# Performance work log

Measured on AMD Instinct MI355X. Metric: run time of the kernel, lower is better.

## Reference

```python
import jax, jax.numpy as jnp
import numpy as np

HEADS = 8
DIM_HEAD = 64
SCALE = DIM_HEAD ** -0.5


def setup_inputs() -> dict:
    key = jax.random.key(0)
    k1, k2, k3, k4 = jax.random.split(key, 4)
    b, dim, l = 4, 256, 2048
    hidden = HEADS * DIM_HEAD  # 512
    x = jax.random.normal(k1, (b, dim, l), dtype=jnp.float32)
    w_qkv = jax.random.normal(k2, (3 * hidden, dim), dtype=jnp.float32) * (dim ** -0.5)
    w_out = jax.random.normal(k3, (dim, hidden), dtype=jnp.float32) * (hidden ** -0.5)
    b_out = jax.random.normal(k4, (dim,), dtype=jnp.float32) * 0.01
    return {"x": x, "w_qkv": w_qkv, "w_out": w_out, "b_out": b_out}


def reference(x, w_qkv, w_out, b_out):
    b, c, l = x.shape
    hidden = HEADS * DIM_HEAD
    # 1x1 conv == pointwise linear over channels
    qkv = jnp.einsum('oc,bcl->bol', w_qkv, x)  # [b, 3*hidden, l]
    q, k, v = jnp.split(qkv, 3, axis=1)
    def to_heads(t):
        return t.reshape(b, HEADS, DIM_HEAD, l)  # b h d l
    q, k, v = to_heads(q), to_heads(k), to_heads(v)
    q = q * SCALE
    sim = jnp.einsum('bhdi,bhdj->bhij', q, k)      # [b, h, l, l]
    attn = jax.nn.softmax(sim, axis=-1)
    out = jnp.einsum('bhij,bhdj->bhid', attn, v)   # [b, h, l, d]
    out = out.transpose(0, 1, 3, 2).reshape(b, hidden, l)  # b (h d) l
    return jnp.einsum('oc,bcl->bol', w_out, out) + b_out[None, :, None]
```

## Files before the change

kernel.cpp:

```cpp
#include <hip/hip_runtime.h>
#include <math.h>

#define Bn   4
#define Cc   256
#define Ll   2048
#define Hh   8
#define Dd   64
#define HID  512
#define OQKV 1536

#define QSCALE 0.18033688011112042f
#define ESHIFT 4.328085122666891f

typedef _Float16 half4v __attribute__((ext_vector_type(4)));
typedef _Float16 half8v __attribute__((ext_vector_type(8)));
typedef __fp16   fp16x2 __attribute__((ext_vector_type(2)));
typedef float    f32x16 __attribute__((ext_vector_type(16)));
typedef unsigned uint2v __attribute__((ext_vector_type(2)));

__device__ __forceinline__ void gload_lds16(const _Float16* g, _Float16* l) {
  __builtin_amdgcn_global_load_lds(
      (const __attribute__((address_space(1))) void*)g,
      (__attribute__((address_space(3))) void*)l, 16, 0, 0);
}

__device__ inline unsigned pkrtz(float a, float b) {
  union { fp16x2 h; unsigned u; } v;
  v.h = __builtin_amdgcn_cvt_pkrtz(a, b);
  return v.u;
}

__global__ __launch_bounds__(256) void conv_xTw(const float* __restrict__ x,
                                                const float* __restrict__ wqkv,
                                                const float* __restrict__ wout,
                                                _Float16* __restrict__ xT,
                                                _Float16* __restrict__ wqkvh,
                                                _Float16* __restrict__ wouth) {
  __shared__ _Float16 T[64][72];
  const int l0 = blockIdx.x * 64, c0 = blockIdx.y * 64, bz = blockIdx.z;
  const int t = threadIdx.x;
  {
    int gid = (((blockIdx.z * gridDim.y + blockIdx.y) * gridDim.x + blockIdx.x) << 8) + t;
    int nthr = (gridDim.x * gridDim.y * gridDim.z) << 8;
    for (int i = gid; i < OQKV * Cc; i += nthr) {
      float v = wqkv[i];
      if (i < HID * Cc) v *= QSCALE;
      wqkvh[i] = (_Float16)v;
    }
    for (int i = gid; i < Cc * HID; i += nthr) wouth[i] = (_Float16)wout[i];
  }
  const float* xb = x + ((size_t)bz * Cc + c0) * Ll + l0;
  {
    int cl = t >> 2, lq = (t & 3) * 16;
#pragma unroll
    for (int i = 0; i < 16; i += 4) {
      float4 v = *(const float4*)&xb[(size_t)cl * Ll + lq + i];
      T[lq + i + 0][cl] = (_Float16)v.x;
      T[lq + i + 1][cl] = (_Float16)v.y;
      T[lq + i + 2][cl] = (_Float16)v.z;
      T[lq + i + 3][cl] = (_Float16)v.w;
    }
  }
  __syncthreads();
  {
    int ll = t >> 2, cq = (t & 3) * 16;
    _Float16* dst = xT + ((size_t)bz * Ll + l0 + ll) * Cc + c0 + cq;
    *(half8v*)&dst[0] = *(const half8v*)&T[ll][cq];
    *(half8v*)&dst[8] = *(const half8v*)&T[ll][cq + 8];
  }
}

template <int MODE>
__global__ __launch_bounds__(256) void gemm64(
    const _Float16* __restrict__ A, const _Float16* __restrict__ B,
    const float* __restrict__ bias, void* __restrict__ C, int M, int K) {
  __shared__ _Float16 As[64][64];
  __shared__ _Float16 Bs[64][64];
  const int bz = blockIdx.z;
  const int m0 = blockIdx.y * 64, n0 = blockIdx.x * 64;
  const int t = threadIdx.x;
  const int w = t >> 6, lane = t & 63, lid = lane & 31, lh = lane >> 5;
  const int mw = (w >> 1) * 32, nw = (w & 1) * 32;
  const _Float16* Bb = B + (size_t)bz * (size_t)Ll * K;
  const int srow = lane >> 3;
  const int sgr  = ((lane & 7) ^ srow) << 3;

  f32x16 acc;
#pragma unroll
  for (int r = 0; r < 16; ++r) acc[r] = 0.0f;

  for (int k0 = 0; k0 < K; k0 += 64) {
#pragma unroll
    for (int q = 0; q < 2; ++q) {
      const int r0 = (q * 4 + w) * 8;
      gload_lds16(&A[(size_t)(m0 + r0 + srow) * K + k0 + sgr], &As[r0][0]);
      gload_lds16(&Bb[(size_t)(n0 + r0 + srow) * K + k0 + sgr], &Bs[r0][0]);
    }
    __syncthreads();
    const int rk = lid & 7;
#pragma unroll
    for (int kq = 0; kq < 4; ++kq) {
      const int co = ((2 * kq + lh) ^ rk) << 3;
      half8v af = *(const half8v*)&As[mw + lid][co];
      half8v bf = *(const half8v*)&Bs[nw + lid][co];
      acc = __builtin_amdgcn_mfma_f32_32x32x16_f16(af, bf, acc, 0, 0, 0);
    }
    __syncthreads();
  }
#pragma unroll
  for (int r = 0; r < 16; ++r) {
    const int row = m0 + mw + (r & 3) + 8 * (r >> 2) + 4 * lh;
    const int col = n0 + nw + lid;
    if (MODE == 1) {
      ((float*)C)[((size_t)bz * M + row) * Ll + col] = acc[r] + bias[row];
    } else {
      ((_Float16*)C)[((size_t)bz * M + row) * Ll + col] = (_Float16)acc[r];
    }
  }
}

__global__ __launch_bounds__(512, 4) void attn_f16(const _Float16* __restrict__ qkv,
                                                   _Float16* __restrict__ aoutT) {
  const int n = blockIdx.x;
  const int xcd = n & 7;
  const int x = (n >> 3) & 15;
  const int gs = n >> 7;
  const int g = gs * 8 + xcd;
  const int h = g & 7, b = g >> 3;
  const int i0 = x * 128;

  const int t = threadIdx.x;
  const int w = t >> 6, lane = t & 63, lid = lane & 31, lh = lane >> 5;
  const int wg = w & 3;
  const int wj = w >> 2;
  const _Float16* qb = qkv + ((size_t)b * OQKV + h * Dd) * Ll;
  const _Float16* kb = qb + (size_t)HID * Ll;
  const _Float16* vb = qb + (size_t)(2 * HID) * Ll;

  __shared__ __align__(16) char lds_raw[55296];
  _Float16 (*Qs)[72]     = (_Float16 (*)[72])(lds_raw);
  _Float16 (*Ks)[64][72] = (_Float16 (*)[64][72])(lds_raw + 18432);
  _Float16 (*Vs)[64][72] = (_Float16 (*)[64][72])(lds_raw + 36864);

  {
    int il = ((t >> 8) << 6) + (t & 15) * 4;
    int dl = ((t >> 4) & 15) * 4;
    int cc = dl >> 3, cs = dl & 7;
    half4v rows[4];
#pragma unroll
    for (int r = 0; r < 4; ++r)
      rows[r] = *(const half4v*)&qb[(size_t)(dl + r) * Ll + i0 + il];
#pragma unroll
    for (int c = 0; c < 4; ++c) {
      half4v o;
      o[0] = rows[0][c]; o[1] = rows[1][c]; o[2] = rows[2][c]; o[3] = rows[3][c];
      int row = il + c;
      *(half4v*)&Qs[row][((cc ^ ((row >> 2) & 7)) << 3) | cs] = o;
    }
  }

  const bool isK = t < 256;
  const int ts = isK ? t : t - 256;
  const int kjl = (ts & 15) * 4, kdl = (ts >> 4) * 4;
  const int kcc = kdl >> 3, kcs = kdl & 7;
  const int vdl = ts >> 2, vjl = (ts & 3) * 16;

  if (isK) {
    half4v rows[4];
#pragma unroll
    for (int r = 0; r < 4; ++r)
      rows[r] = *(const half4v*)&kb[(size_t)(kdl + r) * Ll + kjl];
#pragma unroll
    for (int c = 0; c < 4; ++c) {
      half4v o;
      o[0] = rows[0][c]; o[1] = rows[1][c]; o[2] = rows[2][c]; o[3] = rows[3][c];
      int row = kjl + c;
      *(half4v*)&Ks[0][row][((kcc ^ ((row >> 2) & 7)) << 3) | kcs] = o;
    }
  } else {
    *(half8v*)&Vs[0][vdl][vjl]     = *(const half8v*)&vb[(size_t)vdl * Ll + vjl];
    *(half8v*)&Vs[0][vdl][vjl + 8] = *(const half8v*)&vb[(size_t)vdl * Ll + vjl + 8];
  }
  __syncthreads();

  const int key = (lid >> 2) & 7;
  half8v qf[4];
#pragma unroll
  for (int kq = 0; kq < 4; ++kq)
    qf[kq] = *(const half8v*)&Qs[32 * wg + lid][((2 * kq + lh) ^ key) << 3];

  float lsum = 0.0f;
  f32x16 oacc[2];
#pragma unroll
  for (int ds = 0; ds < 2; ++ds)
#pragma unroll
    for (int r = 0; r < 16; ++r) oacc[ds][r] = 0.0f;

  const int krow = wj * 32 + lid;

  for (int j0 = 0; j0 < Ll; j0 += 64) {
    const int cur = (j0 >> 6) & 1;
    const int nj = j0 + 64;
    const bool more = nj < Ll;

    half4v krows[4];
    half8v vr0, vr1;
    if (more) {
      if (isK) {
#pragma unroll
        for (int r = 0; r < 4; ++r)
          krows[r] = *(const half4v*)&kb[(size_t)(kdl + r) * Ll + nj + kjl];
      } else {
        vr0 = *(const half8v*)&vb[(size_t)vdl * Ll + nj + vjl];
        vr1 = *(const half8v*)&vb[(size_t)vdl * Ll + nj + vjl + 8];
      }
    }

    f32x16 s;
#pragma unroll
    for (int r = 0; r < 16; ++r) s[r] = -ESHIFT;
    __builtin_amdgcn_s_setprio(1);
#pragma unroll
    for (int kq = 0; kq < 4; ++kq) {
      half8v kf = *(const half8v*)&Ks[cur][krow][((2 * kq + lh) ^ key) << 3];
      s = __builtin_amdgcn_mfma_f32_32x32x16_f16(kf, qf[kq], s, 0, 0, 0);
    }
    __builtin_amdgcn_s_setprio(0);
    unsigned W[8];
#pragma unroll
    for (int q = 0; q < 4; ++q) {
      float p0 = __builtin_amdgcn_exp2f(s[4 * q + 0]);
      float p1 = __builtin_amdgcn_exp2f(s[4 * q + 1]);
      float p2 = __builtin_amdgcn_exp2f(s[4 * q + 2]);
      float p3 = __builtin_amdgcn_exp2f(s[4 * q + 3]);
      lsum += (p0 + p1) + (p2 + p3);
      W[2 * q]     = pkrtz(p0, p1);
      W[2 * q + 1] = pkrtz(p2, p3);
    }
#pragma unroll
    for (int f = 0; f < 2; ++f) {
      uint2v r02 = __builtin_amdgcn_permlane32_swap(W[4 * f + 0], W[4 * f + 2], false, false);
      uint2v r13 = __builtin_amdgcn_permlane32_swap(W[4 * f + 1], W[4 * f + 3], false, false);
      union { unsigned u[4]; half8v hv; } pu;
      pu.u[0] = r02[0];
      pu.u[1] = r13[0];
      pu.u[2] = r02[1];
      pu.u[3] = r13[1];
      const int jq = 2 * wj + f;
      __builtin_amdgcn_s_setprio(1);
#pragma unroll
      for (int ds = 0; ds < 2; ++ds) {
        half8v vf = *(const half8v*)&Vs[cur][ds * 32 + lid][jq * 16 + 8 * lh];
        oacc[ds] = __builtin_amdgcn_mfma_f32_32x32x16_f16(vf, pu.hv, oacc[ds], 0, 0, 0);
      }
      __builtin_amdgcn_s_setprio(0);
    }

    if (more) {
      const int nb = cur ^ 1;
      if (isK) {
#pragma unroll
        for (int c = 0; c < 4; ++c) {
          half4v o;
          o[0] = krows[0][c]; o[1] = krows[1][c]; o[2] = krows[2][c]; o[3] = krows[3][c];
          int row = kjl + c;
          *(half4v*)&Ks[nb][row][((kcc ^ ((row >> 2) & 7)) << 3) | kcs] = o;
        }
      } else {
        *(half8v*)&Vs[nb][vdl][vjl]     = vr0;
        *(half8v*)&Vs[nb][vdl][vjl + 8] = vr1;
      }
      __syncthreads();
    }
  }

  lsum += __shfl_xor(lsum, 32);
  __syncthreads();
  float* red = (float*)lds_raw;
  const int rbase = ((wg << 6) + lane) * 33;
  if (wj == 1) {
#pragma unroll
    for (int ds = 0; ds < 2; ++ds)
#pragma unroll
      for (int r = 0; r < 16; ++r) red[rbase + ds * 16 + r] = oacc[ds][r];
    red[rbase + 32] = lsum;
  }
  __syncthreads();
  if (wj == 0) {
#pragma unroll
    for (int ds = 0; ds < 2; ++ds)
#pragma unroll
      for (int r = 0; r < 16; ++r) oacc[ds][r] += red[rbase + ds * 16 + r];
    lsum += red[rbase + 32];
    float inv = 1.0f / lsum;
    _Float16* dst = aoutT + ((size_t)b * Ll + i0 + 32 * wg + lid) * HID + h * Dd;
#pragma unroll
    for (int ds = 0; ds < 2; ++ds)
#pragma unroll
      for (int g2 = 0; g2 < 4; ++g2) {
        int d = ds * 32 + 8 * g2 + 4 * lh;
        half4v o;
#pragma unroll
        for (int c = 0; c < 4; ++c) o[c] = (_Float16)(oacc[ds][4 * g2 + c] * inv);
        *(half4v*)&dst[d] = o;
      }
  }
}

extern "C" void kernel_launch(void* const* d_in, const int* in_sizes, int n_in,
                              void* d_out, int out_size, void* d_ws, size_t ws_size,
                              hipStream_t stream) {
  const float* x     = (const float*)d_in[0];
  const float* w_qkv = (const float*)d_in[1];
  const float* w_out = (const float*)d_in[2];
  const float* b_out = (const float*)d_in[3];
  float* out = (float*)d_out;

  char* ws = (char*)d_ws;
  _Float16* xT     = (_Float16*)(ws);
  _Float16* wqkvh  = (_Float16*)(ws + 4194304);
  _Float16* wouth  = (_Float16*)(ws + 4980736);
  _Float16* qkvh   = (_Float16*)(ws + 5242880);
  _Float16* aoutT  = (_Float16*)(ws + 30408704);

  dim3 blk(256);
  conv_xTw<<<dim3(Ll / 64, Cc / 64, Bn), blk, 0, stream>>>(x, w_qkv, w_out, xT, wqkvh, wouth);
  gemm64<0><<<dim3(Ll / 64, OQKV / 64, Bn), blk, 0, stream>>>(
      wqkvh, xT, nullptr, qkvh, OQKV, Cc);
  attn_f16<<<dim3(512, 1, 1), dim3(512), 0, stream>>>(qkvh, aoutT);
  gemm64<1><<<dim3(Ll / 64, Cc / 64, Bn), blk, 0, stream>>>(
      wouth, aoutT, b_out, out, Cc, HID);
}
```

Baseline: 140.6 us.

## Widen attention blocks to 1024 threads with 128-key tiles and four-way split

```diff
diff --git a/kernel.cpp b/kernel.cpp
--- a/kernel.cpp
+++ b/kernel.cpp
@@ -119,15 +119,19 @@
   }
 }
 
-__global__ __launch_bounds__(512, 4) void attn_f16(const _Float16* __restrict__ qkv,
-                                                   _Float16* __restrict__ aoutT) {
+__global__ __launch_bounds__(1024, 8) void attn_f16(const _Float16* __restrict__ qkv,
+                                                    _Float16* __restrict__ aoutT) {
+  extern __shared__ __align__(16) char lds[];
+  _Float16 (*Ks)[128][72] = (_Float16 (*)[128][72])(lds);
+  _Float16 (*Vs)[64][136] = (_Float16 (*)[64][136])(lds + 36864);
+
   const int n = blockIdx.x;
   const int xcd = n & 7;
-  const int x = (n >> 3) & 15;
+  const int xt = (n >> 3) & 15;
   const int gs = n >> 7;
   const int g = gs * 8 + xcd;
   const int h = g & 7, b = g >> 3;
-  const int i0 = x * 128;
+  const int i0 = xt * 128;
 
   const int t = threadIdx.x;
   const int w = t >> 6, lane = t & 63, lid = lane & 31, lh = lane >> 5;
@@ -137,33 +141,19 @@
   const _Float16* kb = qb + (size_t)HID * Ll;
   const _Float16* vb = qb + (size_t)(2 * HID) * Ll;
 
-  __shared__ __align__(16) char lds_raw[55296];
-  _Float16 (*Qs)[72]     = (_Float16 (*)[72])(lds_raw);
-  _Float16 (*Ks)[64][72] = (_Float16 (*)[64][72])(lds_raw + 18432);
-  _Float16 (*Vs)[64][72] = (_Float16 (*)[64][72])(lds_raw + 36864);
-
-  {
-    int il = ((t >> 8) << 6) + (t & 15) * 4;
-    int dl = ((t >> 4) & 15) * 4;
-    int cc = dl >> 3, cs = dl & 7;
-    half4v rows[4];
-#pragma unroll
-    for (int r = 0; r < 4; ++r)
-      rows[r] = *(const half4v*)&qb[(size_t)(dl + r) * Ll + i0 + il];
-#pragma unroll
-    for (int c = 0; c < 4; ++c) {
-      half4v o;
-      o[0] = rows[0][c]; o[1] = rows[1][c]; o[2] = rows[2][c]; o[3] = rows[3][c];
-      int row = il + c;
-      *(half4v*)&Qs[row][((cc ^ ((row >> 2) & 7)) << 3) | cs] = o;
-    }
-  }
-
-  const bool isK = t < 256;
-  const int ts = isK ? t : t - 256;
-  const int kjl = (ts & 15) * 4, kdl = (ts >> 4) * 4;
+  const int key = (lid >> 2) & 7;
+  half8v qf[4];
+#pragma unroll
+  for (int kq = 0; kq < 4; ++kq)
+#pragma unroll
+    for (int e = 0; e < 8; ++e)
+      qf[kq][e] = qb[(size_t)(kq * 16 + 8 * lh + e) * Ll + i0 + 32 * wg + lid];
+
+  const bool isK = t < 512;
+  const int ts = isK ? t : t - 512;
+  const int kjl = (ts & 31) * 4, kdl = (ts >> 5) * 4;
   const int kcc = kdl >> 3, kcs = kdl & 7;
-  const int vdl = ts >> 2, vjl = (ts & 3) * 16;
+  const int vdl = ts >> 3, vjl = (ts & 7) * 16;
 
   if (isK) {
     half4v rows[4];
@@ -183,12 +173,6 @@
   }
   __syncthreads();
 
-  const int key = (lid >> 2) & 7;
-  half8v qf[4];
-#pragma unroll
-  for (int kq = 0; kq < 4; ++kq)
-    qf[kq] = *(const half8v*)&Qs[32 * wg + lid][((2 * kq + lh) ^ key) << 3];
-
   float lsum = 0.0f;
   f32x16 oacc[2];
 #pragma unroll
@@ -198,9 +182,9 @@
 
   const int krow = wj * 32 + lid;
 
-  for (int j0 = 0; j0 < Ll; j0 += 64) {
-    const int cur = (j0 >> 6) & 1;
-    const int nj = j0 + 64;
+  for (int j0 = 0; j0 < Ll; j0 += 128) {
+    const int cur = (j0 >> 7) & 1;
+    const int nj = j0 + 128;
     const bool more = nj < Ll;
 
     half4v krows[4];
@@ -276,8 +260,26 @@
 
   lsum += __shfl_xor(lsum, 32);
   __syncthreads();
-  float* red = (float*)lds_raw;
+  float* red = (float*)lds;
   const int rbase = ((wg << 6) + lane) * 33;
+  if (wj >= 2) {
+    float* slot = red + (wj - 2) * 8448;
+#pragma unroll
+    for (int ds = 0; ds < 2; ++ds)
+#pragma unroll
+      for (int r = 0; r < 16; ++r) slot[rbase + ds * 16 + r] = oacc[ds][r];
+    slot[rbase + 32] = lsum;
+  }
+  __syncthreads();
+  if (wj < 2) {
+    float* slot = red + wj * 8448;
+#pragma unroll
+    for (int ds = 0; ds < 2; ++ds)
+#pragma unroll
+      for (int r = 0; r < 16; ++r) oacc[ds][r] += slot[rbase + ds * 16 + r];
+    lsum += slot[rbase + 32];
+  }
+  __syncthreads();
   if (wj == 1) {
 #pragma unroll
     for (int ds = 0; ds < 2; ++ds)
@@ -323,11 +325,18 @@
   _Float16* qkvh   = (_Float16*)(ws + 5242880);
   _Float16* aoutT  = (_Float16*)(ws + 30408704);
 
+  static bool lds_cfg = false;
+  if (!lds_cfg) {
+    hipFuncSetAttribute((const void*)attn_f16,
+                        hipFuncAttributeMaxDynamicSharedMemorySize, 71680);
+    lds_cfg = true;
+  }
+
   dim3 blk(256);
   conv_xTw<<<dim3(Ll / 64, Cc / 64, Bn), blk, 0, stream>>>(x, w_qkv, w_out, xT, wqkvh, wouth);
   gemm64<0><<<dim3(Ll / 64, OQKV / 64, Bn), blk, 0, stream>>>(
       wqkvh, xT, nullptr, qkvh, OQKV, Cc);
-  attn_f16<<<dim3(512, 1, 1), dim3(512), 0, stream>>>(qkvh, aoutT);
+  attn_f16<<<dim3(512, 1, 1), dim3(1024), 71680, stream>>>(qkvh, aoutT);
   gemm64<1><<<dim3(Ll / 64, Cc / 64, Bn), blk, 0, stream>>>(
       wouth, aoutT, b_out, out, Cc, HID);
 }
```

Result: slower. 484.5 us (+244.6%).

## Emit Q/K in token-major layout and stream K/V via direct global-to-LDS loads

Applied to the files above, without the earlier changes.

```diff
diff --git a/kernel.cpp b/kernel.cpp
--- a/kernel.cpp
+++ b/kernel.cpp
@@ -70,6 +70,51 @@
   }
 }
 
+__global__ __launch_bounds__(256) void gemmT(const _Float16* __restrict__ xT,
+                                             const _Float16* __restrict__ Wqk,
+                                             _Float16* __restrict__ qkT) {
+  __shared__ _Float16 As[64][64];
+  __shared__ _Float16 Bs[64][64];
+  const int bz = blockIdx.z;
+  const int m0 = blockIdx.y * 64;
+  const int n0 = blockIdx.x * 64;
+  const int t = threadIdx.x;
+  const int w = t >> 6, lane = t & 63, lid = lane & 31, lh = lane >> 5;
+  const int mw = (w >> 1) * 32, nw = (w & 1) * 32;
+  const _Float16* Ab = xT + (size_t)bz * Ll * Cc;
+  const int srow = lane >> 3;
+  const int sgr  = ((lane & 7) ^ srow) << 3;
+
+  f32x16 acc;
+#pragma unroll
+  for (int r = 0; r < 16; ++r) acc[r] = 0.0f;
+
+  for (int k0 = 0; k0 < Cc; k0 += 64) {
+#pragma unroll
+    for (int q = 0; q < 2; ++q) {
+      const int r0 = (q * 4 + w) * 8;
+      gload_lds16(&Ab[(size_t)(m0 + r0 + srow) * Cc + k0 + sgr], &As[r0][0]);
+      gload_lds16(&Wqk[(size_t)(n0 + r0 + srow) * Cc + k0 + sgr], &Bs[r0][0]);
+    }
+    __syncthreads();
+    const int rk = lid & 7;
+#pragma unroll
+    for (int kq = 0; kq < 4; ++kq) {
+      const int co = ((2 * kq + lh) ^ rk) << 3;
+      half8v af = *(const half8v*)&As[mw + lid][co];
+      half8v bf = *(const half8v*)&Bs[nw + lid][co];
+      acc = __builtin_amdgcn_mfma_f32_32x32x16_f16(af, bf, acc, 0, 0, 0);
+    }
+    __syncthreads();
+  }
+#pragma unroll
+  for (int r = 0; r < 16; ++r) {
+    const int row = m0 + mw + (r & 3) + 8 * (r >> 2) + 4 * lh;
+    const int col = n0 + nw + lid;
+    qkT[((size_t)bz * Ll + row) * 1024 + col] = (_Float16)acc[r];
+  }
+}
+
 template <int MODE>
 __global__ __launch_bounds__(256) void gemm64(
     const _Float16* __restrict__ A, const _Float16* __restrict__ B,
@@ -119,75 +164,51 @@
   }
 }
 
-__global__ __launch_bounds__(512, 4) void attn_f16(const _Float16* __restrict__ qkv,
+__global__ __launch_bounds__(512, 4) void attn_f16(const _Float16* __restrict__ qkT,
+                                                   const _Float16* __restrict__ vh,
                                                    _Float16* __restrict__ aoutT) {
+  __shared__ __align__(16) char lds_raw[34816];
+  _Float16 (*Ks)[64][64] = (_Float16 (*)[64][64])(lds_raw);
+  _Float16 (*Vs)[64][64] = (_Float16 (*)[64][64])(lds_raw + 16384);
+
   const int n = blockIdx.x;
   const int xcd = n & 7;
-  const int x = (n >> 3) & 15;
+  const int xt = (n >> 3) & 15;
   const int gs = n >> 7;
   const int g = gs * 8 + xcd;
   const int h = g & 7, b = g >> 3;
-  const int i0 = x * 128;
+  const int i0 = xt * 128;
 
   const int t = threadIdx.x;
   const int w = t >> 6, lane = t & 63, lid = lane & 31, lh = lane >> 5;
   const int wg = w & 3;
   const int wj = w >> 2;
-  const _Float16* qb = qkv + ((size_t)b * OQKV + h * Dd) * Ll;
-  const _Float16* kb = qb + (size_t)HID * Ll;
-  const _Float16* vb = qb + (size_t)(2 * HID) * Ll;
-
-  __shared__ __align__(16) char lds_raw[55296];
-  _Float16 (*Qs)[72]     = (_Float16 (*)[72])(lds_raw);
-  _Float16 (*Ks)[64][72] = (_Float16 (*)[64][72])(lds_raw + 18432);
-  _Float16 (*Vs)[64][72] = (_Float16 (*)[64][72])(lds_raw + 36864);
-
+  const _Float16* qrow  = qkT + (size_t)b * Ll * 1024;
+  const _Float16* kbase = qrow + 512;
+  const _Float16* vbase = vh + ((size_t)b * HID + h * Dd) * Ll;
+
+  half8v qf[4];
   {
-    int il = ((t >> 8) << 6) + (t & 15) * 4;
-    int dl = ((t >> 4) & 15) * 4;
-    int cc = dl >> 3, cs = dl & 7;
-    half4v rows[4];
-#pragma unroll
-    for (int r = 0; r < 4; ++r)
-      rows[r] = *(const half4v*)&qb[(size_t)(dl + r) * Ll + i0 + il];
-#pragma unroll
-    for (int c = 0; c < 4; ++c) {
-      half4v o;
-      o[0] = rows[0][c]; o[1] = rows[1][c]; o[2] = rows[2][c]; o[3] = rows[3][c];
-      int row = il + c;
-      *(half4v*)&Qs[row][((cc ^ ((row >> 2) & 7)) << 3) | cs] = o;
-    }
-  }
-
-  const bool isK = t < 256;
-  const int ts = isK ? t : t - 256;
-  const int kjl = (ts & 15) * 4, kdl = (ts >> 4) * 4;
-  const int kcc = kdl >> 3, kcs = kdl & 7;
-  const int vdl = ts >> 2, vjl = (ts & 3) * 16;
-
-  if (isK) {
-    half4v rows[4];
-#pragma unroll
-    for (int r = 0; r < 4; ++r)
-      rows[r] = *(const half4v*)&kb[(size_t)(kdl + r) * Ll + kjl];
-#pragma unroll
-    for (int c = 0; c < 4; ++c) {
-      half4v o;
-      o[0] = rows[0][c]; o[1] = rows[1][c]; o[2] = rows[2][c]; o[3] = rows[3][c];
-      int row = kjl + c;
-      *(half4v*)&Ks[0][row][((kcc ^ ((row >> 2) & 7)) << 3) | kcs] = o;
-    }
-  } else {
-    *(half8v*)&Vs[0][vdl][vjl]     = *(const half8v*)&vb[(size_t)vdl * Ll + vjl];
-    *(half8v*)&Vs[0][vdl][vjl + 8] = *(const half8v*)&vb[(size_t)vdl * Ll + vjl + 8];
+    const _Float16* q0 = &qrow[(size_t)(i0 + 32 * wg + lid) * 1024 + h * Dd + 8 * lh];
+#pragma unroll
+    for (int kq = 0; kq < 4; ++kq)
+      qf[kq] = *(const half8v*)&q0[kq * 16];
+  }
+
+  const bool isK = w < 4;
+  const int sw = isK ? w : w - 4;
+  const int srow = lane >> 3;
+  const int sgr  = ((lane & 7) ^ srow) << 3;
+
+#pragma unroll
+  for (int q = 0; q < 2; ++q) {
+    const int r0 = (q * 4 + sw) * 8;
+    if (isK)
+      gload_lds16(&kbase[(size_t)(r0 + srow) * 1024 + h * Dd + sgr], &Ks[0][r0][0]);
+    else
+      gload_lds16(&vbase[(size_t)(r0 + srow) * Ll + sgr], &Vs[0][r0][0]);
   }
   __syncthreads();
-
-  const int key = (lid >> 2) & 7;
-  half8v qf[4];
-#pragma unroll
-  for (int kq = 0; kq < 4; ++kq)
-    qf[kq] = *(const half8v*)&Qs[32 * wg + lid][((2 * kq + lh) ^ key) << 3];
 
   float lsum = 0.0f;
   f32x16 oacc[2];
@@ -196,6 +217,7 @@
 #pragma unroll
     for (int r = 0; r < 16; ++r) oacc[ds][r] = 0.0f;
 
+  const int rk = lid & 7;
   const int krow = wj * 32 + lid;
 
   for (int j0 = 0; j0 < Ll; j0 += 64) {
@@ -203,16 +225,15 @@
     const int nj = j0 + 64;
     const bool more = nj < Ll;
 
-    half4v krows[4];
-    half8v vr0, vr1;
     if (more) {
-      if (isK) {
-#pragma unroll
-        for (int r = 0; r < 4; ++r)
-          krows[r] = *(const half4v*)&kb[(size_t)(kdl + r) * Ll + nj + kjl];
-      } else {
-        vr0 = *(const half8v*)&vb[(size_t)vdl * Ll + nj + vjl];
-        vr1 = *(const half8v*)&vb[(size_t)vdl * Ll + nj + vjl + 8];
+      const int nb = cur ^ 1;
+#pragma unroll
+      for (int q = 0; q < 2; ++q) {
+        const int r0 = (q * 4 + sw) * 8;
+        if (isK)
+          gload_lds16(&kbase[(size_t)(nj + r0 + srow) * 1024 + h * Dd + sgr], &Ks[nb][r0][0]);
+        else
+          gload_lds16(&vbase[(size_t)(r0 + srow) * Ll + nj + sgr], &Vs[nb][r0][0]);
       }
     }
 
@@ -222,7 +243,7 @@
     __builtin_amdgcn_s_setprio(1);
 #pragma unroll
     for (int kq = 0; kq < 4; ++kq) {
-      half8v kf = *(const half8v*)&Ks[cur][krow][((2 * kq + lh) ^ key) << 3];
+      half8v kf = *(const half8v*)&Ks[cur][krow][((2 * kq + lh) ^ rk) << 3];
       s = __builtin_amdgcn_mfma_f32_32x32x16_f16(kf, qf[kq], s, 0, 0, 0);
     }
     __builtin_amdgcn_s_setprio(0);
@@ -250,28 +271,13 @@
       __builtin_amdgcn_s_setprio(1);
 #pragma unroll
       for (int ds = 0; ds < 2; ++ds) {
-        half8v vf = *(const half8v*)&Vs[cur][ds * 32 + lid][jq * 16 + 8 * lh];
+        half8v vf = *(const half8v*)&Vs[cur][ds * 32 + lid][((2 * jq + lh) ^ rk) << 3];
         oacc[ds] = __builtin_amdgcn_mfma_f32_32x32x16_f16(vf, pu.hv, oacc[ds], 0, 0, 0);
       }
       __builtin_amdgcn_s_setprio(0);
     }
 
-    if (more) {
-      const int nb = cur ^ 1;
-      if (isK) {
-#pragma unroll
-        for (int c = 0; c < 4; ++c) {
-          half4v o;
-          o[0] = krows[0][c]; o[1] = krows[1][c]; o[2] = krows[2][c]; o[3] = krows[3][c];
-          int row = kjl + c;
-          *(half4v*)&Ks[nb][row][((kcc ^ ((row >> 2) & 7)) << 3) | kcs] = o;
-        }
-      } else {
-        *(half8v*)&Vs[nb][vdl][vjl]     = vr0;
-        *(half8v*)&Vs[nb][vdl][vjl + 8] = vr1;
-      }
-      __syncthreads();
-    }
+    if (more) __syncthreads();
   }
 
   lsum += __shfl_xor(lsum, 32);
@@ -320,14 +326,16 @@
   _Float16* xT     = (_Float16*)(ws);
   _Float16* wqkvh  = (_Float16*)(ws + 4194304);
   _Float16* wouth  = (_Float16*)(ws + 4980736);
-  _Float16* qkvh   = (_Float16*)(ws + 5242880);
+  _Float16* qkT    = (_Float16*)(ws + 5242880);
+  _Float16* vh     = (_Float16*)(ws + 22020096);
   _Float16* aoutT  = (_Float16*)(ws + 30408704);
 
   dim3 blk(256);
   conv_xTw<<<dim3(Ll / 64, Cc / 64, Bn), blk, 0, stream>>>(x, w_qkv, w_out, xT, wqkvh, wouth);
-  gemm64<0><<<dim3(Ll / 64, OQKV / 64, Bn), blk, 0, stream>>>(
-      wqkvh, xT, nullptr, qkvh, OQKV, Cc);
-  attn_f16<<<dim3(512, 1, 1), dim3(512), 0, stream>>>(qkvh, aoutT);
+  gemmT<<<dim3(1024 / 64, Ll / 64, Bn), blk, 0, stream>>>(xT, wqkvh, qkT);
+  gemm64<0><<<dim3(Ll / 64, HID / 64, Bn), blk, 0, stream>>>(
+      wqkvh + (size_t)2 * HID * Cc, xT, nullptr, vh, HID, Cc);
+  attn_f16<<<dim3(512, 1, 1), dim3(512), 0, stream>>>(qkT, vh, aoutT);
   gemm64<1><<<dim3(Ll / 64, Cc / 64, Bn), blk, 0, stream>>>(
       wouth, aoutT, b_out, out, Cc, HID);
 }
```

Result: no change. 140.1 us (-0.4%).
